# Kernel tuning notes

Measured on AMD Instinct MI355X. Metric: run time of the kernel, lower is better.

Reference implementation:

```python
import jax, jax.numpy as jnp
import numpy as np

B, N, D, DEPTH = 1, 512, 128, 4


def mlp_apply(W, x):
    # W: (depth, d, d), x: (..., d). First layer has no activation, then silu before each matmul.
    x = x @ W[0]
    for i in range(1, DEPTH):
        x = jax.nn.silu(x) @ W[i]
    return x


def _binop(x, y):
    # linear recurrence combine: s_t = a_t * s_{t-1} + b_t
    a1, b1 = x
    a2, b2 = y
    return (a1 * a2, a2 * b1 + b2)


def setup_inputs() -> dict:
    key = jax.random.key(0)
    ks = jax.random.split(key, 7)
    s = 0.02  # scale for projection weights (torch Linear-like init magnitude)
    return {
        "seq": jax.random.normal(ks[0], (B, N, D), jnp.float32),
        "W_mem": jax.random.normal(ks[1], (DEPTH, D, D), jnp.float32) * (D ** -0.5),
        "W_q": jax.random.normal(ks[2], (D, D), jnp.float32) * s,
        "W_kv": jax.random.normal(ks[3], (D, 2 * D), jnp.float32) * s,
        "W_mom": jax.random.normal(ks[4], (D, 1), jnp.float32) * s,
        "W_step": jax.random.normal(ks[5], (D, 1), jnp.float32) * s,
        "W_decay": jax.random.normal(ks[6], (D, 1), jnp.float32) * s,
    }


def reference(seq, W_mem, W_q, W_kv, W_mom, W_step, W_decay):
    b, n, d = seq.shape
    # --- store_memories ---
    adaptive_lr = (seq @ W_step)[..., 0]            # (b, n)
    adaptive_mom = seq @ W_mom                      # (b, n, 1)
    decay = jax.nn.sigmoid(seq @ W_decay)           # (b, n, 1)

    kv = seq.reshape(b * n, d) @ W_kv               # (bn, 2d)
    keys, values = kv[:, :d], kv[:, d:]

    def loss_fn(W, k, v):
        pred = mlp_apply(W, k)                      # (d,)
        # (pred - v)^2 .mean(-1).sum() for a single sample == mean over d
        return jnp.mean((pred - v) ** 2)

    # per-sample meta-gradients wrt memory MLP weights
    losses, grads = jax.vmap(jax.value_and_grad(loss_fn, argnums=0), in_axes=(None, 0, 0))(W_mem, keys, values)
    grads = grads.reshape(b, n, DEPTH, d, d)
    surprise = grads * (-adaptive_lr)[..., None, None, None]   # (b,n,depth,d,d)

    # momentum_t = adaptive_mom_t * momentum_{t-1} + surprise_t  (assoc. scan over n)
    am = adaptive_mom[..., None, None]              # (b, n, 1, 1, 1)
    _, momentum = jax.lax.associative_scan(_binop, (am, surprise), axis=1)

    # update_t = (1 - decay_t) * update_{t-1} + momentum_t
    dec = (1.0 - decay)[..., None, None]            # (b, n, 1, 1, 1)
    _, updates = jax.lax.associative_scan(_binop, (dec, momentum), axis=1)

    # --- retrieve_memories with per-token updated weights ---
    q = (seq @ W_q).reshape(b * n, d)
    W_tok = (W_mem[None, None] + updates).reshape(b * n, DEPTH, d, d)
    retrieved = jax.vmap(mlp_apply)(W_tok, q).reshape(b, n, d)
    return retrieved
```

## Files before the change

### kernel.cpp

```cpp
#include <hip/hip_runtime.h>
#include <hip/hip_bf16.h>
#include <math.h>

#define N 512
#define D 128
#define DD (D*D)
#define ND (N*D)
#define LSTR 132
#define CSTR 36

__device__ __forceinline__ float sigmoidf_(float x) { return 1.f / (1.f + expf(-x)); }

__global__ void k_transpose(const float* __restrict__ W_mem, float* __restrict__ WT) {
    int idx = blockIdx.x * 256 + threadIdx.x;
    int l = idx / DD;
    int r = idx % DD;
    int i = r / D;
    int j = r % D;
    WT[idx] = W_mem[(l + 1) * DD + j * D + i];
}

__global__ __launch_bounds__(512) void k_phase1(
    const float* __restrict__ seq, const float* __restrict__ W_mem,
    const float* __restrict__ W_q, const float* __restrict__ W_kv,
    const float* __restrict__ W_mom, const float* __restrict__ W_step,
    const float* __restrict__ W_decay, const float* __restrict__ WT,
    float* __restrict__ Q, float* __restrict__ INS, float* __restrict__ ES,
    float* __restrict__ am, float* __restrict__ dec)
{
    __shared__ float s_seq[D], s_v[D], s_cur[D];
    __shared__ float s_h[4][D];
    __shared__ float s_part[4][D];
    __shared__ float s_p3[4][3][D];
    __shared__ float s_red[8];
    __shared__ float s_lr;

    const int t = blockIdx.x;
    const int tid = threadIdx.x;
    const int j = tid & 127;
    const int p = tid >> 7;
    const int i0 = p * 32;

    if (p == 0) s_seq[j] = seq[t * D + j];
    __syncthreads();

    float ps = 0.f;
    if (p == 1) ps = s_seq[j] * W_step[j];
    else if (p == 2) ps = s_seq[j] * W_mom[j];
    else if (p == 3) ps = s_seq[j] * W_decay[j];
#pragma unroll
    for (int off = 32; off > 0; off >>= 1) ps += __shfl_down(ps, off);
    if ((tid & 63) == 0) s_red[tid >> 6] = ps;
    __syncthreads();
    if (tid == 0) s_lr = s_red[2] + s_red[3];
    else if (tid == 1) am[t] = s_red[4] + s_red[5];
    else if (tid == 2) dec[t] = 1.f - sigmoidf_(s_red[6] + s_red[7]);

    float kp = 0.f, vp = 0.f, qp = 0.f;
#pragma unroll 8
    for (int ii = 0; ii < 32; ii++) {
        int i = i0 + ii;
        float si = s_seq[i];
        kp += si * W_kv[i * 256 + j];
        vp += si * W_kv[i * 256 + 128 + j];
        qp += si * W_q[i * 128 + j];
    }
    s_p3[p][0][j] = kp; s_p3[p][1][j] = vp; s_p3[p][2][j] = qp;
    __syncthreads();
    if (p == 0) {
        float kj = s_p3[0][0][j] + s_p3[1][0][j] + s_p3[2][0][j] + s_p3[3][0][j];
        s_cur[j] = kj;
        INS[t * D + j] = kj;
    } else if (p == 1) {
        s_v[j] = s_p3[0][1][j] + s_p3[1][1][j] + s_p3[2][1][j] + s_p3[3][1][j];
    } else if (p == 2) {
        Q[t * D + j] = s_p3[0][2][j] + s_p3[1][2][j] + s_p3[2][2][j] + s_p3[3][2][j];
    }
    __syncthreads();

    for (int l = 0; l < 4; l++) {
        const float* Wl = W_mem + l * DD;
        float yp = 0.f;
#pragma unroll 8
        for (int ii = 0; ii < 32; ii++) {
            int i = i0 + ii;
            yp += s_cur[i] * Wl[i * D + j];
        }
        s_part[p][j] = yp;
        __syncthreads();
        if (p == 0) {
            float y = s_part[0][j] + s_part[1][j] + s_part[2][j] + s_part[3][j];
            s_h[l][j] = y;
            if (l < 3) {
                float a = y * sigmoidf_(y);
                s_cur[j] = a;
                INS[(l + 1) * ND + t * D + j] = a;
            }
        }
        __syncthreads();
    }

    if (p == 0) {
        float e = -s_lr * (2.f / (float)D) * (s_h[3][j] - s_v[j]);
        ES[3 * ND + t * D + j] = e;
        s_cur[j] = e;
    }
    __syncthreads();

    for (int l = 3; l >= 1; l--) {
        const float* Wt = WT + (l - 1) * DD;
        float gp = 0.f;
#pragma unroll 8
        for (int ii = 0; ii < 32; ii++) {
            int i = i0 + ii;
            gp += s_cur[i] * Wt[i * D + j];
        }
        s_part[p][j] = gp;
        __syncthreads();
        if (p == 0) {
            float g = s_part[0][j] + s_part[1][j] + s_part[2][j] + s_part[3][j];
            float h = s_h[l - 1][j];
            float sg = sigmoidf_(h);
            float e2 = g * (sg * (1.f + h * (1.f - sg)));
            ES[(l - 1) * ND + t * D + j] = e2;
            s_cur[j] = e2;
        }
        __syncthreads();
    }
}

__global__ __launch_bounds__(512) void k_logscan(
    const float* __restrict__ am, const float* __restrict__ dec,
    double* __restrict__ LA, double* __restrict__ LDp, int* __restrict__ NC)
{
    __shared__ double sa[N], sd[N];
    __shared__ int sn[N];
    const int t = threadIdx.x;
    float a = am[t];
    float d = dec[t];
    sa[t] = log((double)fmaxf(fabsf(a), 1e-38f));
    sd[t] = log((double)fmaxf(d, 1e-38f));
    sn[t] = (a < 0.f) ? 1 : 0;
    __syncthreads();
    for (int off = 1; off < N; off <<= 1) {
        double va = 0.0, vd = 0.0; int vn = 0;
        if (t >= off) { va = sa[t - off]; vd = sd[t - off]; vn = sn[t - off]; }
        __syncthreads();
        sa[t] += va; sd[t] += vd; sn[t] += vn;
        __syncthreads();
    }
    LA[t] = sa[t]; LDp[t] = sd[t]; NC[t] = sn[t];
}

__global__ __launch_bounds__(256) void k_build(
    const double* __restrict__ LA, const double* __restrict__ LDp,
    const int* __restrict__ NC,
    float* __restrict__ Amat, float* __restrict__ Dmat)
{
    int idx = blockIdx.x * 256 + threadIdx.x;
    int u = idx >> 9;
    int s = idx & (N - 1);
    float va = 0.f, vd = 0.f;
    if (s <= u) {
        va = expf((float)(LA[u] - LA[s]));
        if ((NC[u] - NC[s]) & 1) va = -va;
        vd = expf((float)(LDp[u] - LDp[s]));
    }
    Amat[idx] = va;
    Dmat[idx] = vd;
}

__global__ __launch_bounds__(256) void k_betamm(
    const float* __restrict__ Dmat, const float* __restrict__ Amat,
    float* __restrict__ beta)
{
    const int bs = blockIdx.x;
    const int bt = blockIdx.y;
    const int z  = blockIdx.z;
    if (bs > bt) return;
    const int span = bt - bs + 1;
    const int chunk = (span + 3) >> 2;
    const int kBeg = bs + z * chunk;
    const int kEnd = (kBeg + chunk < bt + 1) ? (kBeg + chunk) : (bt + 1);
    if (kBeg >= kEnd) return;

    __shared__ float sD[32][33];
    __shared__ float sA[32][33];

    const int tx = threadIdx.x & 31;
    const int ty = threadIdx.x >> 5;
    float acc[4] = {0.f, 0.f, 0.f, 0.f};

    for (int kt = kBeg; kt < kEnd; kt++) {
        for (int i = threadIdx.x; i < 1024; i += 256) {
            int r = i >> 5, c = i & 31;
            sD[r][c] = Dmat[(bt * 32 + r) * N + kt * 32 + c];
            sA[r][c] = Amat[(kt * 32 + r) * N + bs * 32 + c];
        }
        __syncthreads();
#pragma unroll 8
        for (int k = 0; k < 32; k++) {
            float a = sA[k][tx];
#pragma unroll
            for (int j = 0; j < 4; j++)
                acc[j] += sD[ty + 8 * j][k] * a;
        }
        __syncthreads();
    }
#pragma unroll
    for (int j = 0; j < 4; j++)
        atomicAdd(&beta[(bt * 32 + ty + 8 * j) * N + bs * 32 + tx], acc[j]);
}

__global__ __launch_bounds__(64) void k_layer(
    const float* __restrict__ Xin, float* __restrict__ Yout,
    const float* __restrict__ Wl, const float* __restrict__ INSl,
    const float* __restrict__ ESl, const float* __restrict__ beta,
    int actIn)
{
    const int r = blockIdx.x;
    const int z = blockIdx.y;
    const int t0 = r * 16;
    const int lane = threadIdx.x;
    const bool isW = (z >= 17);
    if (!isW && z > (r >> 1)) return;

    __shared__ float sX[16 * LSTR];
    __shared__ float sI[32 * LSTR];
    __shared__ float sE[32 * LSTR];
    __shared__ float sc[16 * CSTR];

#pragma unroll
    for (int i = 0; i < 8; i++) {
        int f4 = lane + 64 * i;
        int row = f4 >> 5, c4 = f4 & 31;
        float4 v = ((const float4*)(Xin + t0 * D))[f4];
        if (actIn) {
            v.x = v.x * sigmoidf_(v.x); v.y = v.y * sigmoidf_(v.y);
            v.z = v.z * sigmoidf_(v.z); v.w = v.w * sigmoidf_(v.w);
        }
        *(float4*)(sX + row * LSTR + c4 * 4) = v;
    }

    if (isW) {
        __syncthreads();
        const int k0 = (z - 17) * 64;
        const int ti0 = (lane >> 4) * 4;
        const int jA = (lane & 15) * 4;
        float acc[4][8];
#pragma unroll
        for (int a = 0; a < 4; a++)
#pragma unroll
            for (int b = 0; b < 8; b++) acc[a][b] = 0.f;

#pragma unroll 4
        for (int k = k0; k < k0 + 64; k++) {
            float4 w0 = *(const float4*)(Wl + k * D + jA);
            float4 w1 = *(const float4*)(Wl + k * D + 64 + jA);
            float xv[4];
#pragma unroll
            for (int a = 0; a < 4; a++) xv[a] = sX[(ti0 + a) * LSTR + k];
#pragma unroll
            for (int a = 0; a < 4; a++) {
                acc[a][0] += xv[a] * w0.x; acc[a][1] += xv[a] * w0.y;
                acc[a][2] += xv[a] * w0.z; acc[a][3] += xv[a] * w0.w;
                acc[a][4] += xv[a] * w1.x; acc[a][5] += xv[a] * w1.y;
                acc[a][6] += xv[a] * w1.z; acc[a][7] += xv[a] * w1.w;
            }
        }
#pragma unroll
        for (int a = 0; a < 4; a++) {
            float* yp = Yout + (t0 + ti0 + a) * D;
#pragma unroll
            for (int q = 0; q < 4; q++) {
                atomicAdd(yp + jA + q,      acc[a][q]);
                atomicAdd(yp + 64 + jA + q, acc[a][4 + q]);
            }
        }
        return;
    }

    const int s0 = z * 32;
#pragma unroll
    for (int i = 0; i < 16; i++) {
        int f4 = lane + 64 * i;
        int row = f4 >> 5, c4 = f4 & 31;
        float4 a = ((const float4*)(INSl + s0 * D))[f4];
        float4 b = ((const float4*)(ESl + s0 * D))[f4];
        *(float4*)(sI + row * LSTR + c4 * 4) = a;
        *(float4*)(sE + row * LSTR + c4 * 4) = b;
    }
    __syncthreads();

    const int tiA = (lane >> 3) * 2;
    const int siA = lane & 7;
    float g1[2][4];
#pragma unroll
    for (int v = 0; v < 2; v++)
#pragma unroll
        for (int u = 0; u < 4; u++) g1[v][u] = 0.f;

    for (int k4 = 0; k4 < D; k4 += 4) {
        float4 a0 = *(float4*)(sX + tiA * LSTR + k4);
        float4 a1 = *(float4*)(sX + (tiA + 1) * LSTR + k4);
#pragma unroll
        for (int u = 0; u < 4; u++) {
            float4 b = *(float4*)(sI + (siA + 8 * u) * LSTR + k4);
            g1[0][u] += a0.x * b.x + a0.y * b.y + a0.z * b.z + a0.w * b.w;
            g1[1][u] += a1.x * b.x + a1.y * b.y + a1.z * b.z + a1.w * b.w;
        }
    }
#pragma unroll
    for (int v = 0; v < 2; v++)
#pragma unroll
        for (int u = 0; u < 4; u++) {
            int ti = tiA + v, si = siA + 8 * u;
            sc[ti * CSTR + si] = g1[v][u] * beta[(t0 + ti) * N + s0 + si];
        }
    __syncthreads();

    const int ti0 = (lane >> 4) * 4;
    const int jA = (lane & 15) * 4;
    float acc[4][8];
#pragma unroll
    for (int a = 0; a < 4; a++)
#pragma unroll
        for (int b = 0; b < 8; b++) acc[a][b] = 0.f;

    for (int s4 = 0; s4 < 32; s4 += 4) {
        float cva[4][4];
#pragma unroll
        for (int a = 0; a < 4; a++)
            *(float4*)cva[a] = *(float4*)(sc + (ti0 + a) * CSTR + s4);
#pragma unroll
        for (int u = 0; u < 4; u++) {
            float4 e0 = *(float4*)(sE + (s4 + u) * LSTR + jA);
            float4 e1 = *(float4*)(sE + (s4 + u) * LSTR + 64 + jA);
#pragma unroll
            for (int a = 0; a < 4; a++) {
                float cu = cva[a][u];
                acc[a][0] += cu * e0.x; acc[a][1] += cu * e0.y;
                acc[a][2] += cu * e0.z; acc[a][3] += cu * e0.w;
                acc[a][4] += cu * e1.x; acc[a][5] += cu * e1.y;
                acc[a][6] += cu * e1.z; acc[a][7] += cu * e1.w;
            }
        }
    }
#pragma unroll
    for (int a = 0; a < 4; a++) {
        float* yp = Yout + (t0 + ti0 + a) * D;
#pragma unroll
        for (int q = 0; q < 4; q++) {
            atomicAdd(yp + jA + q,      acc[a][q]);
            atomicAdd(yp + 64 + jA + q, acc[a][4 + q]);
        }
    }
}

extern "C" void kernel_launch(void* const* d_in, const int* in_sizes, int n_in,
                              void* d_out, int out_size, void* d_ws, size_t ws_size,
                              hipStream_t stream) {
    const float* seq     = (const float*)d_in[0];
    const float* W_mem   = (const float*)d_in[1];
    const float* W_q     = (const float*)d_in[2];
    const float* W_kv    = (const float*)d_in[3];
    const float* W_mom   = (const float*)d_in[4];
    const float* W_step  = (const float*)d_in[5];
    const float* W_decay = (const float*)d_in[6];
    float* out = (float*)d_out;

    float* ws   = (float*)d_ws;
    float* am   = ws;
    float* dec  = am + N;
    float* Q    = dec + N;
    float* INS  = Q + ND;
    float* ES   = INS + 4 * ND;
    float* beta = ES + 4 * ND;
    float* Y012 = beta + N * N;
    float* WT   = Y012 + 3 * ND;
    float* Amat = WT + 3 * DD;
    float* Dmat = Amat + N * N;
    double* LA  = (double*)(Dmat + N * N);
    double* LDp = LA + N;
    int* NC     = (int*)(LDp + N);

    hipMemsetAsync(beta, 0, (N * N + 3 * ND) * sizeof(float), stream);
    hipMemsetAsync(out, 0, ND * sizeof(float), stream);

    k_transpose<<<192, 256, 0, stream>>>(W_mem, WT);
    k_phase1<<<N, 512, 0, stream>>>(seq, W_mem, W_q, W_kv, W_mom, W_step, W_decay,
                                    WT, Q, INS, ES, am, dec);
    k_logscan<<<1, N, 0, stream>>>(am, dec, LA, LDp, NC);
    k_build<<<(N * N) / 256, 256, 0, stream>>>(LA, LDp, NC, Amat, Dmat);
    dim3 mmgrid(N / 32, N / 32, 4);
    k_betamm<<<mmgrid, 256, 0, stream>>>(Dmat, Amat, beta);

    float* Y0 = Y012;
    float* Y1 = Y012 + ND;
    float* Y2 = Y012 + 2 * ND;
    dim3 lgrid(32, 19);
    k_layer<<<lgrid, 64, 0, stream>>>(Q,  Y0,  W_mem,          INS,          ES,          beta, 0);
    k_layer<<<lgrid, 64, 0, stream>>>(Y0, Y1,  W_mem + DD,     INS + ND,     ES + ND,     beta, 1);
    k_layer<<<lgrid, 64, 0, stream>>>(Y1, Y2,  W_mem + 2 * DD, INS + 2 * ND, ES + 2 * ND, beta, 1);
    k_layer<<<lgrid, 64, 0, stream>>>(Y2, out, W_mem + 3 * DD, INS + 3 * ND, ES + 3 * ND, beta, 1);
}
```

Measured before the change: 186.3 us.

## Fuse decay-matrix build into beta matmul and widen layer blocks to 256 threads

Removes the k_build kernel and the Amat/Dmat buffers. The betamm kernel now computes the decay and momentum coefficient tiles on the fly from the log-scan prefix arrays, which saves one launch and two N×N global write/read round trips at the cost of recomputing exps per tile. The k_layer kernel goes from 64 to 256 threads per block with one output row per thread group, giving less register tiling per thread but more parallelism per block. It also prefetches beta before the barrier.

```diff
diff --git a/kernel.cpp b/kernel.cpp
--- a/kernel.cpp
+++ b/kernel.cpp
@@ -152,27 +152,9 @@
     LA[t] = sa[t]; LDp[t] = sd[t]; NC[t] = sn[t];
 }
 
-__global__ __launch_bounds__(256) void k_build(
+__global__ __launch_bounds__(256) void k_betamm(
     const double* __restrict__ LA, const double* __restrict__ LDp,
-    const int* __restrict__ NC,
-    float* __restrict__ Amat, float* __restrict__ Dmat)
-{
-    int idx = blockIdx.x * 256 + threadIdx.x;
-    int u = idx >> 9;
-    int s = idx & (N - 1);
-    float va = 0.f, vd = 0.f;
-    if (s <= u) {
-        va = expf((float)(LA[u] - LA[s]));
-        if ((NC[u] - NC[s]) & 1) va = -va;
-        vd = expf((float)(LDp[u] - LDp[s]));
-    }
-    Amat[idx] = va;
-    Dmat[idx] = vd;
-}
-
-__global__ __launch_bounds__(256) void k_betamm(
-    const float* __restrict__ Dmat, const float* __restrict__ Amat,
-    float* __restrict__ beta)
+    const int* __restrict__ NC, float* __restrict__ beta)
 {
     const int bs = blockIdx.x;
     const int bt = blockIdx.y;
@@ -194,8 +176,15 @@
     for (int kt = kBeg; kt < kEnd; kt++) {
         for (int i = threadIdx.x; i < 1024; i += 256) {
             int r = i >> 5, c = i & 31;
-            sD[r][c] = Dmat[(bt * 32 + r) * N + kt * 32 + c];
-            sA[r][c] = Amat[(kt * 32 + r) * N + bs * 32 + c];
+            int u1 = bt * 32 + r, s1 = kt * 32 + c;
+            sD[r][c] = (s1 <= u1) ? expf((float)(LDp[u1] - LDp[s1])) : 0.f;
+            int u2 = kt * 32 + r, s2 = bs * 32 + c;
+            float va = 0.f;
+            if (s2 <= u2) {
+                va = expf((float)(LA[u2] - LA[s2]));
+                if ((NC[u2] - NC[s2]) & 1) va = -va;
+            }
+            sA[r][c] = va;
         }
         __syncthreads();
 #pragma unroll 8
@@ -212,7 +201,7 @@
         atomicAdd(&beta[(bt * 32 + ty + 8 * j) * N + bs * 32 + tx], acc[j]);
 }
 
-__global__ __launch_bounds__(64) void k_layer(
+__global__ __launch_bounds__(256) void k_layer(
     const float* __restrict__ Xin, float* __restrict__ Yout,
     const float* __restrict__ Wl, const float* __restrict__ INSl,
     const float* __restrict__ ESl, const float* __restrict__ beta,
@@ -231,8 +220,8 @@
     __shared__ float sc[16 * CSTR];
 
 #pragma unroll
-    for (int i = 0; i < 8; i++) {
-        int f4 = lane + 64 * i;
+    for (int i = 0; i < 2; i++) {
+        int f4 = lane + 256 * i;
         int row = f4 >> 5, c4 = f4 & 31;
         float4 v = ((const float4*)(Xin + t0 * D))[f4];
         if (actIn) {
@@ -242,119 +231,77 @@
         *(float4*)(sX + row * LSTR + c4 * 4) = v;
     }
 
+    const int ti = lane >> 4;
+    const int q15 = lane & 15;
+
     if (isW) {
         __syncthreads();
         const int k0 = (z - 17) * 64;
-        const int ti0 = (lane >> 4) * 4;
-        const int jA = (lane & 15) * 4;
-        float acc[4][8];
-#pragma unroll
-        for (int a = 0; a < 4; a++)
-#pragma unroll
-            for (int b = 0; b < 8; b++) acc[a][b] = 0.f;
-
+        const int j8 = q15 * 8;
+        float acc[8];
+#pragma unroll
+        for (int b = 0; b < 8; b++) acc[b] = 0.f;
 #pragma unroll 4
         for (int k = k0; k < k0 + 64; k++) {
-            float4 w0 = *(const float4*)(Wl + k * D + jA);
-            float4 w1 = *(const float4*)(Wl + k * D + 64 + jA);
-            float xv[4];
-#pragma unroll
-            for (int a = 0; a < 4; a++) xv[a] = sX[(ti0 + a) * LSTR + k];
-#pragma unroll
-            for (int a = 0; a < 4; a++) {
-                acc[a][0] += xv[a] * w0.x; acc[a][1] += xv[a] * w0.y;
-                acc[a][2] += xv[a] * w0.z; acc[a][3] += xv[a] * w0.w;
-                acc[a][4] += xv[a] * w1.x; acc[a][5] += xv[a] * w1.y;
-                acc[a][6] += xv[a] * w1.z; acc[a][7] += xv[a] * w1.w;
-            }
-        }
-#pragma unroll
-        for (int a = 0; a < 4; a++) {
-            float* yp = Yout + (t0 + ti0 + a) * D;
-#pragma unroll
-            for (int q = 0; q < 4; q++) {
-                atomicAdd(yp + jA + q,      acc[a][q]);
-                atomicAdd(yp + 64 + jA + q, acc[a][4 + q]);
-            }
-        }
+            float4 w0 = *(const float4*)(Wl + k * D + j8);
+            float4 w1 = *(const float4*)(Wl + k * D + j8 + 4);
+            float xv = sX[ti * LSTR + k];
+            acc[0] += xv * w0.x; acc[1] += xv * w0.y;
+            acc[2] += xv * w0.z; acc[3] += xv * w0.w;
+            acc[4] += xv * w1.x; acc[5] += xv * w1.y;
+            acc[6] += xv * w1.z; acc[7] += xv * w1.w;
+        }
+        float* yp = Yout + (t0 + ti) * D + j8;
+#pragma unroll
+        for (int q = 0; q < 8; q++) atomicAdd(yp + q, acc[q]);
         return;
     }
 
     const int s0 = z * 32;
 #pragma unroll
-    for (int i = 0; i < 16; i++) {
-        int f4 = lane + 64 * i;
+    for (int i = 0; i < 4; i++) {
+        int f4 = lane + 256 * i;
         int row = f4 >> 5, c4 = f4 & 31;
         float4 a = ((const float4*)(INSl + s0 * D))[f4];
         float4 b = ((const float4*)(ESl + s0 * D))[f4];
         *(float4*)(sI + row * LSTR + c4 * 4) = a;
         *(float4*)(sE + row * LSTR + c4 * 4) = b;
     }
-    __syncthreads();
-
-    const int tiA = (lane >> 3) * 2;
-    const int siA = lane & 7;
-    float g1[2][4];
-#pragma unroll
-    for (int v = 0; v < 2; v++)
-#pragma unroll
-        for (int u = 0; u < 4; u++) g1[v][u] = 0.f;
-
+    const int si0 = q15 * 2;
+    float b0 = beta[(t0 + ti) * N + s0 + si0];
+    float b1 = beta[(t0 + ti) * N + s0 + si0 + 1];
+    __syncthreads();
+
+    float g0 = 0.f, g1 = 0.f;
+#pragma unroll 8
     for (int k4 = 0; k4 < D; k4 += 4) {
-        float4 a0 = *(float4*)(sX + tiA * LSTR + k4);
-        float4 a1 = *(float4*)(sX + (tiA + 1) * LSTR + k4);
-#pragma unroll
-        for (int u = 0; u < 4; u++) {
-            float4 b = *(float4*)(sI + (siA + 8 * u) * LSTR + k4);
-            g1[0][u] += a0.x * b.x + a0.y * b.y + a0.z * b.z + a0.w * b.w;
-            g1[1][u] += a1.x * b.x + a1.y * b.y + a1.z * b.z + a1.w * b.w;
-        }
-    }
-#pragma unroll
-    for (int v = 0; v < 2; v++)
-#pragma unroll
-        for (int u = 0; u < 4; u++) {
-            int ti = tiA + v, si = siA + 8 * u;
-            sc[ti * CSTR + si] = g1[v][u] * beta[(t0 + ti) * N + s0 + si];
-        }
-    __syncthreads();
-
-    const int ti0 = (lane >> 4) * 4;
-    const int jA = (lane & 15) * 4;
-    float acc[4][8];
-#pragma unroll
-    for (int a = 0; a < 4; a++)
-#pragma unroll
-        for (int b = 0; b < 8; b++) acc[a][b] = 0.f;
-
-    for (int s4 = 0; s4 < 32; s4 += 4) {
-        float cva[4][4];
-#pragma unroll
-        for (int a = 0; a < 4; a++)
-            *(float4*)cva[a] = *(float4*)(sc + (ti0 + a) * CSTR + s4);
-#pragma unroll
-        for (int u = 0; u < 4; u++) {
-            float4 e0 = *(float4*)(sE + (s4 + u) * LSTR + jA);
-            float4 e1 = *(float4*)(sE + (s4 + u) * LSTR + 64 + jA);
-#pragma unroll
-            for (int a = 0; a < 4; a++) {
-                float cu = cva[a][u];
-                acc[a][0] += cu * e0.x; acc[a][1] += cu * e0.y;
-                acc[a][2] += cu * e0.z; acc[a][3] += cu * e0.w;
-                acc[a][4] += cu * e1.x; acc[a][5] += cu * e1.y;
-                acc[a][6] += cu * e1.z; acc[a][7] += cu * e1.w;
-            }
-        }
-    }
-#pragma unroll
-    for (int a = 0; a < 4; a++) {
-        float* yp = Yout + (t0 + ti0 + a) * D;
-#pragma unroll
-        for (int q = 0; q < 4; q++) {
-            atomicAdd(yp + jA + q,      acc[a][q]);
-            atomicAdd(yp + 64 + jA + q, acc[a][4 + q]);
-        }
-    }
+        float4 a  = *(float4*)(sX + ti * LSTR + k4);
+        float4 p0 = *(float4*)(sI + si0 * LSTR + k4);
+        float4 p1 = *(float4*)(sI + (si0 + 1) * LSTR + k4);
+        g0 += a.x * p0.x + a.y * p0.y + a.z * p0.z + a.w * p0.w;
+        g1 += a.x * p1.x + a.y * p1.y + a.z * p1.z + a.w * p1.w;
+    }
+    sc[ti * CSTR + si0]     = g0 * b0;
+    sc[ti * CSTR + si0 + 1] = g1 * b1;
+    __syncthreads();
+
+    const int j8 = q15 * 8;
+    float acc[8];
+#pragma unroll
+    for (int b = 0; b < 8; b++) acc[b] = 0.f;
+#pragma unroll 8
+    for (int s = 0; s < 32; s++) {
+        float cv = sc[ti * CSTR + s];
+        float4 e0 = *(float4*)(sE + s * LSTR + j8);
+        float4 e1 = *(float4*)(sE + s * LSTR + j8 + 4);
+        acc[0] += cv * e0.x; acc[1] += cv * e0.y;
+        acc[2] += cv * e0.z; acc[3] += cv * e0.w;
+        acc[4] += cv * e1.x; acc[5] += cv * e1.y;
+        acc[6] += cv * e1.z; acc[7] += cv * e1.w;
+    }
+    float* yp = Yout + (t0 + ti) * D + j8;
+#pragma unroll
+    for (int q = 0; q < 8; q++) atomicAdd(yp + q, acc[q]);
 }
 
 extern "C" void kernel_launch(void* const* d_in, const int* in_sizes, int n_in,
@@ -378,9 +325,7 @@
     float* beta = ES + 4 * ND;
     float* Y012 = beta + N * N;
     float* WT   = Y012 + 3 * ND;
-    float* Amat = WT + 3 * DD;
-    float* Dmat = Amat + N * N;
-    double* LA  = (double*)(Dmat + N * N);
+    double* LA  = (double*)(WT + 3 * DD);
     double* LDp = LA + N;
     int* NC     = (int*)(LDp + N);
 
@@ -391,16 +336,15 @@
     k_phase1<<<N, 512, 0, stream>>>(seq, W_mem, W_q, W_kv, W_mom, W_step, W_decay,
                                     WT, Q, INS, ES, am, dec);
     k_logscan<<<1, N, 0, stream>>>(am, dec, LA, LDp, NC);
-    k_build<<<(N * N) / 256, 256, 0, stream>>>(LA, LDp, NC, Amat, Dmat);
     dim3 mmgrid(N / 32, N / 32, 4);
-    k_betamm<<<mmgrid, 256, 0, stream>>>(Dmat, Amat, beta);
+    k_betamm<<<mmgrid, 256, 0, stream>>>(LA, LDp, NC, beta);
 
     float* Y0 = Y012;
     float* Y1 = Y012 + ND;
     float* Y2 = Y012 + 2 * ND;
     dim3 lgrid(32, 19);
-    k_layer<<<lgrid, 64, 0, stream>>>(Q,  Y0,  W_mem,          INS,          ES,          beta, 0);
-    k_layer<<<lgrid, 64, 0, stream>>>(Y0, Y1,  W_mem + DD,     INS + ND,     ES + ND,     beta, 1);
-    k_layer<<<lgrid, 64, 0, stream>>>(Y1, Y2,  W_mem + 2 * DD, INS + 2 * ND, ES + 2 * ND, beta, 1);
-    k_layer<<<lgrid, 64, 0, stream>>>(Y2, out, W_mem + 3 * DD, INS + 3 * ND, ES + 3 * ND, beta, 1);
-}
+    k_layer<<<lgrid, 256, 0, stream>>>(Q,  Y0,  W_mem,          INS,          ES,          beta, 0);
+    k_layer<<<lgrid, 256, 0, stream>>>(Y0, Y1,  W_mem + DD,     INS + ND,     ES + ND,     beta, 1);
+    k_layer<<<lgrid, 256, 0, stream>>>(Y1, Y2,  W_mem + 2 * DD, INS + 2 * ND, ES + 2 * ND, beta, 1);
+    k_layer<<<lgrid, 256, 0, stream>>>(Y2, out, W_mem + 3 * DD, INS + 3 * ND, ES + 3 * ND, beta, 1);
+}
```

Result: slower. 218.7 us (+17.4%).
